# Kernel tuning notes

Measured on AMD Instinct MI355X. Metric: run time of the kernel, lower is better.

Reference implementation:

```python
import jax, jax.numpy as jnp
import numpy as np

N_NODES = 100000


def gcn_conv(x, W, b, edge_index, n):
    """PyG-style GCNConv: x' = D^-1/2 (A+I) D^-1/2 (x W) + b."""
    loop = jnp.arange(n, dtype=edge_index.dtype)
    src = jnp.concatenate([edge_index[0], loop])
    dst = jnp.concatenate([edge_index[1], loop])
    deg = jax.ops.segment_sum(jnp.ones_like(dst, dtype=x.dtype), dst, num_segments=n)
    dinv = jax.lax.rsqrt(deg)  # deg >= 1 because of self-loops
    norm = dinv[src] * dinv[dst]  # [E+N]
    h = x @ W  # [N, out]
    msg = h[src] * norm[:, None]  # gather + scale
    return jax.ops.segment_sum(msg, dst, num_segments=n) + b


def edge_logits(z, edge_index, We, be):
    # concat(src_emb, dst_emb) @ We + be, without materializing the concat twice
    d = z.shape[1]
    return z[edge_index[0]] @ We[:d] + z[edge_index[1]] @ We[d:] + be


def setup_inputs() -> dict:
    key = jax.random.key(0)
    ks = jax.random.split(key, 10)
    x = jax.random.normal(ks[0], (N_NODES, 512), dtype=jnp.float32)
    edge_index = jax.random.randint(ks[1], (2, 3200000), 0, N_NODES, dtype=jnp.int64)
    pos_edge_index = jax.random.randint(ks[2], (2, 1000000), 0, N_NODES, dtype=jnp.int64)
    neg_edge_index = jax.random.randint(ks[3], (2, 1000000), 0, N_NODES, dtype=jnp.int64)
    s1 = 1.0 / np.sqrt(512)
    s2 = 1.0 / np.sqrt(16)
    se = 1.0 / np.sqrt(128)
    W1 = jax.random.uniform(ks[4], (512, 16), jnp.float32, -s1, s1)
    b1 = jnp.zeros((16,), jnp.float32)
    W2 = jax.random.uniform(ks[5], (16, 64), jnp.float32, -s2, s2)
    b2 = jnp.zeros((64,), jnp.float32)
    We = jax.random.uniform(ks[6], (128, 1), jnp.float32, -se, se)  # 2*num_classes -> 1
    be = jnp.zeros((1,), jnp.float32)
    return {"x": x, "W1": W1, "b1": b1, "W2": W2, "b2": b2, "We": We, "be": be,
            "edge_index": edge_index, "pos_edge_index": pos_edge_index,
            "neg_edge_index": neg_edge_index}


def reference(x, W1, b1, W2, b2, We, be, edge_index, pos_edge_index, neg_edge_index):
    n = x.shape[0]
    h = jax.nn.relu(gcn_conv(x, W1, b1, edge_index, n))
    z = gcn_conv(h, W2, b2, edge_index, n)  # node embeddings [N, num_classes]
    pos = edge_logits(z, pos_edge_index, We, be)
    neg = edge_logits(z, neg_edge_index, We, be)
    return z, jnp.concatenate([pos, neg], axis=0)
```

## Files before the change

### kernel.cpp

```cpp
#include <hip/hip_runtime.h>
#include <hip/hip_bf16.h>


constexpr int TPB = 256;
constexpr int LOG_W = 7;
constexpr int W_BKT = 128;
constexpr int NB_MAX = 1024;
constexpr int CAP = 5120;
constexpr int EPB = 8192;

__global__ __launch_bounds__(256) void scatterA_kernel(const int* __restrict__ src,
                                                       const int* __restrict__ dst,
                                                       int* __restrict__ bcursor,
                                                       int* __restrict__ pairs,
                                                       int E, int NB) {
    __shared__ int hist[NB_MAX];
    __shared__ int lstart[NB_MAX];
    __shared__ int gbase[NB_MAX];
    __shared__ int lcur[NB_MAX];
    __shared__ int csum[256];
    __shared__ int val[EPB];
    __shared__ unsigned short bkt[EPB];
    const int t = threadIdx.x;
    const int e0 = blockIdx.x * EPB;
    const int cnt = min(EPB, E - e0);

    for (int i = t; i < NB; i += 256) hist[i] = 0;
    __syncthreads();
    for (int i = t; i < cnt; i += 256) atomicAdd(&hist[dst[e0 + i] >> LOG_W], 1);
    __syncthreads();

    int loc[4], tsum = 0;
#pragma unroll
    for (int j = 0; j < 4; ++j) {
        int idx = t * 4 + j;
        int v = (idx < NB) ? hist[idx] : 0;
        loc[j] = tsum; tsum += v;
    }
    csum[t] = tsum;
    __syncthreads();
    for (int off = 1; off < 256; off <<= 1) {
        int v = (t >= off) ? csum[t - off] : 0;
        __syncthreads();
        csum[t] += v;
        __syncthreads();
    }
    int cbase = (t > 0) ? csum[t - 1] : 0;
#pragma unroll
    for (int j = 0; j < 4; ++j) {
        int idx = t * 4 + j;
        if (idx < NB) lstart[idx] = cbase + loc[j];
    }
    __syncthreads();
    for (int b = t; b < NB; b += 256) {
        gbase[b] = hist[b] ? atomicAdd(&bcursor[b], hist[b]) : 0;
        lcur[b] = lstart[b];
    }
    __syncthreads();
    for (int i = t; i < cnt; i += 256) {
        int s = src[e0 + i], d = dst[e0 + i];
        int b = d >> LOG_W;
        int p = atomicAdd(&lcur[b], 1);
        val[p] = ((d & (W_BKT - 1)) << 17) | s;
        bkt[p] = (unsigned short)b;
    }
    __syncthreads();
    for (int i = t; i < cnt; i += 256) {
        int b = bkt[i];
        int ofs = gbase[b] + (i - lstart[b]);
        if (ofs < CAP) pairs[(size_t)b * CAP + ofs] = val[i];
    }
}

__global__ __launch_bounds__(256) void bucketB_kernel(const int* __restrict__ bcursor,
                                                      int* __restrict__ pairs,
                                                      float* __restrict__ dinv,
                                                      int* __restrict__ row_start,
                                                      int* __restrict__ row_end,
                                                      int N) {
    __shared__ int cnt[W_BKT];
    __shared__ int scn[W_BKT];
    __shared__ int cur[W_BKT];
    __shared__ int img[CAP];
    const int b = blockIdx.x;
    const int t = threadIdx.x;
    const int len = min(bcursor[b], CAP);
    const int n0 = b * W_BKT;
    int* p = pairs + (size_t)b * CAP;

    if (t < W_BKT) cnt[t] = 0;
    __syncthreads();
    for (int i = t; i < len; i += 256) atomicAdd(&cnt[p[i] >> 17], 1);
    __syncthreads();
    if (t < W_BKT) scn[t] = cnt[t];
    __syncthreads();
    for (int off = 1; off < W_BKT; off <<= 1) {
        int v = (t < W_BKT && t >= off) ? scn[t - off] : 0;
        __syncthreads();
        if (t < W_BKT) scn[t] += v;
        __syncthreads();
    }
    if (t < W_BKT) {
        int c = cnt[t];
        int es = scn[t] - c;
        cur[t] = es;
        int n = n0 + t;
        if (n < N) {
            dinv[n] = rsqrtf((float)(c + 1));
            int rs = b * CAP + es;
            row_start[n] = rs;
            row_end[n] = rs + c;
        }
    }
    __syncthreads();
    for (int i = t; i < len; i += 256) {
        int v = p[i];
        int r = atomicAdd(&cur[v >> 17], 1);
        img[r] = v & 0x1FFFF;
    }
    __syncthreads();
    for (int i = t; i < len; i += 256) p[i] = img[i];
}

__global__ __launch_bounds__(256) void gemm1_kernel(const float* __restrict__ x,
                                                    const float* __restrict__ W1,
                                                    const float* __restrict__ dinv,
                                                    float* __restrict__ xs, int N) {
    __shared__ float buf[512 * 16];
    const int t = threadIdx.x;
    {
        const float4* w4 = (const float4*)W1;
        float4* b4 = (float4*)buf;
        for (int i = t; i < 2048; i += 256) b4[i] = w4[i];
    }
    __syncthreads();

    const int r = t & 63, q = t >> 6;
    const int row = blockIdx.x * 64 + r;
    const bool valid = row < N;
    const float* xrow = x + (size_t)row * 512 + q * 128;

    float acc[16];
#pragma unroll
    for (int c = 0; c < 16; ++c) acc[c] = 0.0f;

    if (valid) {
        const int kb = q * 128;
#pragma unroll 2
        for (int k0 = 0; k0 < 128; k0 += 16) {
            const float4* xp = (const float4*)(xrow + k0);
            float4 a0 = xp[0], a1 = xp[1], a2 = xp[2], a3 = xp[3];
            float xv[16] = {a0.x, a0.y, a0.z, a0.w, a1.x, a1.y, a1.z, a1.w,
                            a2.x, a2.y, a2.z, a2.w, a3.x, a3.y, a3.z, a3.w};
#pragma unroll
            for (int kk = 0; kk < 16; ++kk) {
                const float4* wr = (const float4*)(buf + (kb + k0 + kk) * 16);
                float4 w0 = wr[0], w1 = wr[1], w2 = wr[2], w3 = wr[3];
                float xvk = xv[kk];
                acc[0]  += xvk * w0.x; acc[1]  += xvk * w0.y; acc[2]  += xvk * w0.z; acc[3]  += xvk * w0.w;
                acc[4]  += xvk * w1.x; acc[5]  += xvk * w1.y; acc[6]  += xvk * w1.z; acc[7]  += xvk * w1.w;
                acc[8]  += xvk * w2.x; acc[9]  += xvk * w2.y; acc[10] += xvk * w2.z; acc[11] += xvk * w2.w;
                acc[12] += xvk * w3.x; acc[13] += xvk * w3.y; acc[14] += xvk * w3.z; acc[15] += xvk * w3.w;
            }
        }
    }
    __syncthreads();

    float* red = buf;
    if (q > 0) {
        float4* d0 = (float4*)(red + ((q - 1) * 64 + r) * 16);
        d0[0] = make_float4(acc[0], acc[1], acc[2], acc[3]);
        d0[1] = make_float4(acc[4], acc[5], acc[6], acc[7]);
        d0[2] = make_float4(acc[8], acc[9], acc[10], acc[11]);
        d0[3] = make_float4(acc[12], acc[13], acc[14], acc[15]);
    }
    __syncthreads();
    if (q == 0 && valid) {
#pragma unroll
        for (int p = 0; p < 3; ++p) {
            const float* sr = red + (p * 64 + r) * 16;
#pragma unroll
            for (int c = 0; c < 16; ++c) acc[c] += sr[c];
        }
        float di = dinv[row];
        float4* o = (float4*)(xs + (size_t)row * 16);
        o[0] = make_float4(acc[0] * di, acc[1] * di, acc[2] * di, acc[3] * di);
        o[1] = make_float4(acc[4] * di, acc[5] * di, acc[6] * di, acc[7] * di);
        o[2] = make_float4(acc[8] * di, acc[9] * di, acc[10] * di, acc[11] * di);
        o[3] = make_float4(acc[12] * di, acc[13] * di, acc[14] * di, acc[15] * di);
    }
}

__global__ __launch_bounds__(256) void gather1_kernel(const float* __restrict__ xs,
                                                      const int* __restrict__ csr,
                                                      const int* __restrict__ row_start,
                                                      const int* __restrict__ row_end,
                                                      const float* __restrict__ dinv,
                                                      const float* __restrict__ b1,
                                                      float* __restrict__ hs, int N) {
    int t = threadIdx.x;
    int node = blockIdx.x * 16 + (t >> 4);
    int lane = t & 15;
    if (node >= N) return;
    int rs = row_start[node], re = row_end[node];
    float acc = xs[(size_t)node * 16 + lane];

    int e0 = rs;
    for (; e0 + 16 <= re; e0 += 16) {
        int idx = csr[e0 + lane];
        float v[16];
#pragma unroll
        for (int j = 0; j < 16; ++j) {
            int s = __shfl(idx, j, 16);
            v[j] = xs[(size_t)s * 16 + lane];
        }
#pragma unroll
        for (int j = 0; j < 16; ++j) acc += v[j];
    }
    if (e0 < re) {
        int idx = (e0 + lane < re) ? csr[e0 + lane] : 0;
        int m = re - e0;
        float v[16];
#pragma unroll
        for (int j = 0; j < 16; ++j) {
            int s = __shfl(idx, j, 16);
            v[j] = 0.0f;
            if (j < m) v[j] = xs[(size_t)s * 16 + lane];
        }
#pragma unroll
        for (int j = 0; j < 16; ++j) acc += v[j];
    }

    float di = dinv[node];
    float h = fmaxf(fmaf(di, acc, b1[lane]), 0.0f);
    hs[(size_t)node * 16 + lane] = h * di;
}

__global__ __launch_bounds__(256) void gather2_fin2_kernel(const float* __restrict__ hs,
                                                           const int* __restrict__ csr,
                                                           const int* __restrict__ row_start,
                                                           const int* __restrict__ row_end,
                                                           const float* __restrict__ dinv,
                                                           const float* __restrict__ W2,
                                                           const float* __restrict__ b2,
                                                           const float* __restrict__ We,
                                                           float* __restrict__ z,
                                                           float* __restrict__ s1,
                                                           float* __restrict__ s2, int N) {
    __shared__ float u[16][17];
    __shared__ float w2l[16 * 64];
    __shared__ float wel[128];
    __shared__ float b2l[64];
    int t = threadIdx.x;
    for (int i = t; i < 1024; i += 256) w2l[i] = W2[i];
    if (t < 128) wel[t] = We[t];
    if (t < 64) b2l[t] = b2[t];
    int g = t >> 4, lane = t & 15;
    int node = blockIdx.x * 16 + g;
    if (node < N) {
        int rs = row_start[node], re = row_end[node];
        float acc = hs[(size_t)node * 16 + lane];

        int e0 = rs;
        for (; e0 + 16 <= re; e0 += 16) {
            int idx = csr[e0 + lane];
            float v[16];
#pragma unroll
            for (int j = 0; j < 16; ++j) {
                int s = __shfl(idx, j, 16);
                v[j] = hs[(size_t)s * 16 + lane];
            }
#pragma unroll
            for (int j = 0; j < 16; ++j) acc += v[j];
        }
        if (e0 < re) {
            int idx = (e0 + lane < re) ? csr[e0 + lane] : 0;
            int m = re - e0;
            float v[16];
#pragma unroll
            for (int j = 0; j < 16; ++j) {
                int s = __shfl(idx, j, 16);
                v[j] = 0.0f;
                if (j < m) v[j] = hs[(size_t)s * 16 + lane];
            }
#pragma unroll
            for (int j = 0; j < 16; ++j) acc += v[j];
        }

        u[g][lane] = acc * dinv[node];
    }
    __syncthreads();
    if (node >= N) return;
    int c0 = lane * 4;
    float z0 = b2l[c0], z1 = b2l[c0 + 1], z2 = b2l[c0 + 2], z3 = b2l[c0 + 3];
#pragma unroll
    for (int k = 0; k < 16; ++k) {
        float uk = u[g][k];
        const float* wr = &w2l[k * 64 + c0];
        z0 = fmaf(uk, wr[0], z0);
        z1 = fmaf(uk, wr[1], z1);
        z2 = fmaf(uk, wr[2], z2);
        z3 = fmaf(uk, wr[3], z3);
    }
    float p1 = z0 * wel[c0] + z1 * wel[c0 + 1] + z2 * wel[c0 + 2] + z3 * wel[c0 + 3];
    float p2 = z0 * wel[64 + c0] + z1 * wel[64 + c0 + 1] + z2 * wel[64 + c0 + 2] + z3 * wel[64 + c0 + 3];
#pragma unroll
    for (int off = 1; off < 16; off <<= 1) {
        p1 += __shfl_xor(p1, off, 16);
        p2 += __shfl_xor(p2, off, 16);
    }
    ((float4*)(z + (size_t)node * 64))[lane] = make_float4(z0, z1, z2, z3);
    if (lane == 0) { s1[node] = p1; s2[node] = p2; }
}

__global__ void logits_kernel(const int* __restrict__ src, const int* __restrict__ dst,
                              const float* __restrict__ s1, const float* __restrict__ s2,
                              const float* __restrict__ be, float* __restrict__ out, int E) {
    int e = blockIdx.x * blockDim.x + threadIdx.x;
    if (e >= E) return;
    out[e] = s1[src[e]] + s2[dst[e]] + be[0];
}

extern "C" void kernel_launch(void* const* d_in, const int* in_sizes, int n_in,
                              void* d_out, int out_size, void* d_ws, size_t ws_size,
                              hipStream_t stream) {
    const float* x  = (const float*)d_in[0];
    const float* W1 = (const float*)d_in[1];
    const float* b1 = (const float*)d_in[2];
    const float* W2 = (const float*)d_in[3];
    const float* b2 = (const float*)d_in[4];
    const float* We = (const float*)d_in[5];
    const float* be = (const float*)d_in[6];
    const int* ei   = (const int*)d_in[7];
    const int* pei  = (const int*)d_in[8];
    const int* nei  = (const int*)d_in[9];

    const int N  = in_sizes[0] / 512;
    const int E  = in_sizes[7] / 2;
    const int EP = in_sizes[8] / 2;
    const int EN = in_sizes[9] / 2;
    const int NB = (N + W_BKT - 1) >> LOG_W;

    const int* src  = ei;
    const int* dst  = ei + E;
    const int* psrc = pei;
    const int* pdst = pei + EP;
    const int* nsrc = nei;
    const int* ndst = nei + EN;

    int* wsp = (int*)d_ws;
    int*   bcursor   = wsp;
    float* dinv      = (float*)(wsp + NB_MAX);
    int*   row_start = (int*)(dinv + N);
    int*   row_end   = row_start + N;
    float* s1        = (float*)(row_end + N);
    float* s2        = s1 + N;
    float* xs        = s2 + N;
    float* hs        = xs + (size_t)16 * N;
    int*   pairs     = (int*)(hs + (size_t)16 * N);

    float* z_out = (float*)d_out;
    float* logit_out = z_out + (size_t)64 * N;

    hipMemsetAsync(bcursor, 0, NB_MAX * sizeof(int), stream);

    int gA  = (E + EPB - 1) / EPB;
    int g16 = (N + 15) / 16;
    int g64 = (N + 63) / 64;

    scatterA_kernel<<<gA, TPB, 0, stream>>>(src, dst, bcursor, pairs, E, NB);
    bucketB_kernel<<<NB, TPB, 0, stream>>>(bcursor, pairs, dinv, row_start, row_end, N);

    gemm1_kernel<<<g64, TPB, 0, stream>>>(x, W1, dinv, xs, N);

    gather1_kernel<<<g16, TPB, 0, stream>>>(xs, pairs, row_start, row_end, dinv, b1, hs, N);
    gather2_fin2_kernel<<<g16, TPB, 0, stream>>>(hs, pairs, row_start, row_end, dinv,
                                                 W2, b2, We, z_out, s1, s2, N);

    int gP = (EP + TPB - 1) / TPB;
    int gNeg = (EN + TPB - 1) / TPB;
    logits_kernel<<<gP, TPB, 0, stream>>>(psrc, pdst, s1, s2, be, logit_out, EP);
    logits_kernel<<<gNeg, TPB, 0, stream>>>(nsrc, ndst, s1, s2, be, logit_out + EP, EN);
}
```

Before: 480.7 us.

## Store intermediate node features in fp16, use nontemporal loads, merge logits launches

Stores the intermediate per-node features xs and hs as fp16 instead of fp32, which halves the bytes moved by the random-access gathers in both aggregation passes. The x stream in the GEMM and the edge-index streams in the logits kernel now use nontemporal loads and stores. The two logits launches are merged into one, and the shared-memory staging in gather2 is replaced by shuffles. Rounding to fp16 adds precision error to the aggregated values, and the headroom of fp16 range is not checked.

```diff
diff --git a/kernel.cpp b/kernel.cpp
--- a/kernel.cpp
+++ b/kernel.cpp
@@ -1,5 +1,6 @@
 #include <hip/hip_runtime.h>
 #include <hip/hip_bf16.h>
+#include <hip/hip_fp16.h>
 
 
 constexpr int TPB = 256;
@@ -8,6 +9,8 @@
 constexpr int NB_MAX = 1024;
 constexpr int CAP = 5120;
 constexpr int EPB = 8192;
+
+typedef float f4v __attribute__((ext_vector_type(4)));
 
 __global__ __launch_bounds__(256) void scatterA_kernel(const int* __restrict__ src,
                                                        const int* __restrict__ dst,
@@ -125,7 +128,7 @@
 __global__ __launch_bounds__(256) void gemm1_kernel(const float* __restrict__ x,
                                                     const float* __restrict__ W1,
                                                     const float* __restrict__ dinv,
-                                                    float* __restrict__ xs, int N) {
+                                                    __half* __restrict__ xs, int N) {
     __shared__ float buf[512 * 16];
     const int t = threadIdx.x;
     {
@@ -148,10 +151,13 @@
         const int kb = q * 128;
 #pragma unroll 2
         for (int k0 = 0; k0 < 128; k0 += 16) {
-            const float4* xp = (const float4*)(xrow + k0);
-            float4 a0 = xp[0], a1 = xp[1], a2 = xp[2], a3 = xp[3];
-            float xv[16] = {a0.x, a0.y, a0.z, a0.w, a1.x, a1.y, a1.z, a1.w,
-                            a2.x, a2.y, a2.z, a2.w, a3.x, a3.y, a3.z, a3.w};
+            const f4v* xp = (const f4v*)(xrow + k0);
+            f4v a0 = __builtin_nontemporal_load(xp);
+            f4v a1 = __builtin_nontemporal_load(xp + 1);
+            f4v a2 = __builtin_nontemporal_load(xp + 2);
+            f4v a3 = __builtin_nontemporal_load(xp + 3);
+            float xv[16] = {a0[0], a0[1], a0[2], a0[3], a1[0], a1[1], a1[2], a1[3],
+                            a2[0], a2[1], a2[2], a2[3], a3[0], a3[1], a3[2], a3[3]};
 #pragma unroll
             for (int kk = 0; kk < 16; ++kk) {
                 const float4* wr = (const float4*)(buf + (kb + k0 + kk) * 16);
@@ -183,27 +189,28 @@
             for (int c = 0; c < 16; ++c) acc[c] += sr[c];
         }
         float di = dinv[row];
+        __half hv[16];
+#pragma unroll
+        for (int c = 0; c < 16; ++c) hv[c] = __float2half_rn(acc[c] * di);
         float4* o = (float4*)(xs + (size_t)row * 16);
-        o[0] = make_float4(acc[0] * di, acc[1] * di, acc[2] * di, acc[3] * di);
-        o[1] = make_float4(acc[4] * di, acc[5] * di, acc[6] * di, acc[7] * di);
-        o[2] = make_float4(acc[8] * di, acc[9] * di, acc[10] * di, acc[11] * di);
-        o[3] = make_float4(acc[12] * di, acc[13] * di, acc[14] * di, acc[15] * di);
-    }
-}
-
-__global__ __launch_bounds__(256) void gather1_kernel(const float* __restrict__ xs,
+        o[0] = *(const float4*)&hv[0];
+        o[1] = *(const float4*)&hv[8];
+    }
+}
+
+__global__ __launch_bounds__(256) void gather1_kernel(const __half* __restrict__ xs,
                                                       const int* __restrict__ csr,
                                                       const int* __restrict__ row_start,
                                                       const int* __restrict__ row_end,
                                                       const float* __restrict__ dinv,
                                                       const float* __restrict__ b1,
-                                                      float* __restrict__ hs, int N) {
+                                                      __half* __restrict__ hs, int N) {
     int t = threadIdx.x;
     int node = blockIdx.x * 16 + (t >> 4);
     int lane = t & 15;
     if (node >= N) return;
     int rs = row_start[node], re = row_end[node];
-    float acc = xs[(size_t)node * 16 + lane];
+    float acc = __half2float(xs[(size_t)node * 16 + lane]);
 
     int e0 = rs;
     for (; e0 + 16 <= re; e0 += 16) {
@@ -212,7 +219,7 @@
 #pragma unroll
         for (int j = 0; j < 16; ++j) {
             int s = __shfl(idx, j, 16);
-            v[j] = xs[(size_t)s * 16 + lane];
+            v[j] = __half2float(xs[(size_t)s * 16 + lane]);
         }
 #pragma unroll
         for (int j = 0; j < 16; ++j) acc += v[j];
@@ -225,7 +232,7 @@
         for (int j = 0; j < 16; ++j) {
             int s = __shfl(idx, j, 16);
             v[j] = 0.0f;
-            if (j < m) v[j] = xs[(size_t)s * 16 + lane];
+            if (j < m) v[j] = __half2float(xs[(size_t)s * 16 + lane]);
         }
 #pragma unroll
         for (int j = 0; j < 16; ++j) acc += v[j];
@@ -233,10 +240,10 @@
 
     float di = dinv[node];
     float h = fmaxf(fmaf(di, acc, b1[lane]), 0.0f);
-    hs[(size_t)node * 16 + lane] = h * di;
-}
-
-__global__ __launch_bounds__(256) void gather2_fin2_kernel(const float* __restrict__ hs,
+    hs[(size_t)node * 16 + lane] = __float2half_rn(h * di);
+}
+
+__global__ __launch_bounds__(256) void gather2_fin2_kernel(const __half* __restrict__ hs,
                                                            const int* __restrict__ csr,
                                                            const int* __restrict__ row_start,
                                                            const int* __restrict__ row_end,
@@ -247,7 +254,6 @@
                                                            float* __restrict__ z,
                                                            float* __restrict__ s1,
                                                            float* __restrict__ s2, int N) {
-    __shared__ float u[16][17];
     __shared__ float w2l[16 * 64];
     __shared__ float wel[128];
     __shared__ float b2l[64];
@@ -255,47 +261,48 @@
     for (int i = t; i < 1024; i += 256) w2l[i] = W2[i];
     if (t < 128) wel[t] = We[t];
     if (t < 64) b2l[t] = b2[t];
+    __syncthreads();
+
     int g = t >> 4, lane = t & 15;
     int node = blockIdx.x * 16 + g;
-    if (node < N) {
-        int rs = row_start[node], re = row_end[node];
-        float acc = hs[(size_t)node * 16 + lane];
-
-        int e0 = rs;
-        for (; e0 + 16 <= re; e0 += 16) {
-            int idx = csr[e0 + lane];
-            float v[16];
-#pragma unroll
-            for (int j = 0; j < 16; ++j) {
-                int s = __shfl(idx, j, 16);
-                v[j] = hs[(size_t)s * 16 + lane];
-            }
-#pragma unroll
-            for (int j = 0; j < 16; ++j) acc += v[j];
-        }
-        if (e0 < re) {
-            int idx = (e0 + lane < re) ? csr[e0 + lane] : 0;
-            int m = re - e0;
-            float v[16];
-#pragma unroll
-            for (int j = 0; j < 16; ++j) {
-                int s = __shfl(idx, j, 16);
-                v[j] = 0.0f;
-                if (j < m) v[j] = hs[(size_t)s * 16 + lane];
-            }
-#pragma unroll
-            for (int j = 0; j < 16; ++j) acc += v[j];
-        }
-
-        u[g][lane] = acc * dinv[node];
-    }
-    __syncthreads();
     if (node >= N) return;
+
+    int rs = row_start[node], re = row_end[node];
+    float acc = __half2float(hs[(size_t)node * 16 + lane]);
+
+    int e0 = rs;
+    for (; e0 + 16 <= re; e0 += 16) {
+        int idx = csr[e0 + lane];
+        float v[16];
+#pragma unroll
+        for (int j = 0; j < 16; ++j) {
+            int s = __shfl(idx, j, 16);
+            v[j] = __half2float(hs[(size_t)s * 16 + lane]);
+        }
+#pragma unroll
+        for (int j = 0; j < 16; ++j) acc += v[j];
+    }
+    if (e0 < re) {
+        int idx = (e0 + lane < re) ? csr[e0 + lane] : 0;
+        int m = re - e0;
+        float v[16];
+#pragma unroll
+        for (int j = 0; j < 16; ++j) {
+            int s = __shfl(idx, j, 16);
+            v[j] = 0.0f;
+            if (j < m) v[j] = __half2float(hs[(size_t)s * 16 + lane]);
+        }
+#pragma unroll
+        for (int j = 0; j < 16; ++j) acc += v[j];
+    }
+
+    float uv = acc * dinv[node];
+
     int c0 = lane * 4;
     float z0 = b2l[c0], z1 = b2l[c0 + 1], z2 = b2l[c0 + 2], z3 = b2l[c0 + 3];
 #pragma unroll
     for (int k = 0; k < 16; ++k) {
-        float uk = u[g][k];
+        float uk = __shfl(uv, k, 16);
         const float* wr = &w2l[k * 64 + c0];
         z0 = fmaf(uk, wr[0], z0);
         z1 = fmaf(uk, wr[1], z1);
@@ -313,12 +320,23 @@
     if (lane == 0) { s1[node] = p1; s2[node] = p2; }
 }
 
-__global__ void logits_kernel(const int* __restrict__ src, const int* __restrict__ dst,
+__global__ void logits_kernel(const int* __restrict__ psrc, const int* __restrict__ pdst,
+                              const int* __restrict__ nsrc, const int* __restrict__ ndst,
                               const float* __restrict__ s1, const float* __restrict__ s2,
-                              const float* __restrict__ be, float* __restrict__ out, int E) {
+                              const float* __restrict__ be, float* __restrict__ out,
+                              int EP, int ET) {
     int e = blockIdx.x * blockDim.x + threadIdx.x;
-    if (e >= E) return;
-    out[e] = s1[src[e]] + s2[dst[e]] + be[0];
+    if (e >= ET) return;
+    int s, d;
+    if (e < EP) {
+        s = __builtin_nontemporal_load(psrc + e);
+        d = __builtin_nontemporal_load(pdst + e);
+    } else {
+        s = __builtin_nontemporal_load(nsrc + (e - EP));
+        d = __builtin_nontemporal_load(ndst + (e - EP));
+    }
+    float r = s1[s] + s2[d] + be[0];
+    __builtin_nontemporal_store(r, out + e);
 }
 
 extern "C" void kernel_launch(void* const* d_in, const int* in_sizes, int n_in,
@@ -355,8 +373,8 @@
     int*   row_end   = row_start + N;
     float* s1        = (float*)(row_end + N);
     float* s2        = s1 + N;
-    float* xs        = s2 + N;
-    float* hs        = xs + (size_t)16 * N;
+    __half* xs       = (__half*)(s2 + N);
+    __half* hs       = xs + (size_t)16 * N;
     int*   pairs     = (int*)(hs + (size_t)16 * N);
 
     float* z_out = (float*)d_out;
@@ -377,8 +395,8 @@
     gather2_fin2_kernel<<<g16, TPB, 0, stream>>>(hs, pairs, row_start, row_end, dinv,
                                                  W2, b2, We, z_out, s1, s2, N);
 
-    int gP = (EP + TPB - 1) / TPB;
-    int gNeg = (EN + TPB - 1) / TPB;
-    logits_kernel<<<gP, TPB, 0, stream>>>(psrc, pdst, s1, s2, be, logit_out, EP);
-    logits_kernel<<<gNeg, TPB, 0, stream>>>(nsrc, ndst, s1, s2, be, logit_out + EP, EN);
-}
+    int ET = EP + EN;
+    int gL = (ET + TPB - 1) / TPB;
+    logits_kernel<<<gL, TPB, 0, stream>>>(psrc, pdst, nsrc, ndst, s1, s2, be,
+                                          logit_out, EP, ET);
+}
```

Result: slower. 533.1 us (+10.9%).
